# Optimization experiments

Measured on AMD Instinct MI355X. Metric: run time of the kernel, lower is better.

Reference implementation:

```python
import jax, jax.numpy as jnp
import numpy as np
import math

B, F, T = 32, 512, 4000
H, DK, DV = 8, 64, 64

def setup_inputs() -> dict:
    key = jax.random.key(0)
    ks = jax.random.split(key, 8)
    x = jax.random.normal(ks[0], (B, F, T), dtype=jnp.float32)
    weights = jax.random.randint(ks[1], (B, T), 0, 2, dtype=jnp.int32)
    # learned params
    q = jax.random.normal(ks[2], (H, DK), dtype=jnp.float32) / math.sqrt(DK)  # (1,H,1,dk) squeezed
    lim_k = 1.0 / math.sqrt(F)
    Wk = jax.random.uniform(ks[3], (H * DK, F), minval=-lim_k, maxval=lim_k, dtype=jnp.float32)
    bk = jax.random.uniform(ks[4], (H * DK,), minval=-lim_k, maxval=lim_k, dtype=jnp.float32)
    Wv = jax.random.uniform(ks[5], (H * DV, F), minval=-lim_k, maxval=lim_k, dtype=jnp.float32)
    bv = jax.random.uniform(ks[6], (H * DV,), minval=-lim_k, maxval=lim_k, dtype=jnp.float32)
    return {"x": x, "weights": weights, "q": q, "Wk": Wk, "bk": bk, "Wv": Wv, "bv": bv}

def reference(x, weights, q, Wk, bk, Wv, bv):
    # x: (B, F, T) -> transpose to (B, T, F) since dim=-1
    xt = jnp.swapaxes(x, 1, 2)                                  # (B,T,F)
    k = (xt @ Wk.T + bk).reshape(B, T, H, DK)                   # (B,T,H,dk)
    v = (xt @ Wv.T + bv).reshape(B, T, H, DV)                   # (B,T,H,dv)
    # scores: q (H,dk) dot k -> (B,H,T), scaled
    scores = jnp.einsum('hd,bthd->bht', q, k) / math.sqrt(DK)
    mask = (weights == 0)[:, None, :]                           # (B,1,T)
    scores = jnp.where(mask, jnp.float32(-1e30), scores)
    attn = jax.nn.softmax(scores, axis=-1)
    attn = jnp.where(mask, 0.0, attn)                           # (B,H,T)
    out = jnp.einsum('bht,bthv->bhv', attn, v)                  # (B,H,dv)
    return out.reshape(B, H * DV)                               # keepdim=False
```

## Files before the change

### kernel.cpp

```cpp
#include <hip/hip_runtime.h>
#include <math.h>

#define BB 32
#define FF 512
#define TT 4000
#define HH 8
#define DKK 64
#define DVV 64
#define NT4 1000

__global__ __launch_bounds__(256) void prep_qk(const float* __restrict__ q,
                                               const float* __restrict__ Wk,
                                               const float* __restrict__ bk,
                                               float* __restrict__ qk,
                                               float* __restrict__ qb) {
    int gid = blockIdx.x * 256 + threadIdx.x;
    int h = gid >> 9, f = gid & 511;
    float s = 0.f;
#pragma unroll 8
    for (int d = 0; d < DKK; ++d)
        s += q[h * DKK + d] * Wk[(size_t)(h * DKK + d) * FF + f];
    qk[gid] = s * 0.125f;
    if (gid < HH) {
        float sb = 0.f;
        for (int d = 0; d < DKK; ++d) sb += q[gid * DKK + d] * bk[gid * DKK + d];
        qb[gid] = sb * 0.125f;
    }
}

__global__ __launch_bounds__(256) void prep_wvt(const float* __restrict__ Wv,
                                                float* __restrict__ WvT) {
    int gid = blockIdx.x * 256 + threadIdx.x;
    int hv = gid >> 9, f = gid & 511;
    WvT[f * 512 + hv] = Wv[gid];
}

__global__ __launch_bounds__(256) void k_scores(const float* __restrict__ x,
                                                const float* __restrict__ qk,
                                                const float* __restrict__ qb,
                                                float* __restrict__ sc) {
    __shared__ float4 part[HH * 4 * 64];
    int b = blockIdx.y, tt = blockIdx.x;
    int tid = threadIdx.x, w = tid >> 6, l = tid & 63;
    int t0 = tt << 8;
    int t = t0 + (l << 2);
    float4 acc[HH];
#pragma unroll
    for (int h = 0; h < HH; ++h) acc[h] = make_float4(0.f, 0.f, 0.f, 0.f);
    if (t < TT) {
        const float* xp = x + (size_t)b * FF * TT + t;
        int f40 = w * 32;
        for (int f4 = f40; f4 < f40 + 32; ++f4) {
            int f = f4 << 2;
            float4 xv0 = *(const float4*)(xp + (size_t)(f + 0) * TT);
            float4 xv1 = *(const float4*)(xp + (size_t)(f + 1) * TT);
            float4 xv2 = *(const float4*)(xp + (size_t)(f + 2) * TT);
            float4 xv3 = *(const float4*)(xp + (size_t)(f + 3) * TT);
#pragma unroll
            for (int h = 0; h < HH; ++h) {
                float4 qv = *(const float4*)(qk + h * FF + f);
                acc[h].x += qv.x * xv0.x + qv.y * xv1.x + qv.z * xv2.x + qv.w * xv3.x;
                acc[h].y += qv.x * xv0.y + qv.y * xv1.y + qv.z * xv2.y + qv.w * xv3.y;
                acc[h].z += qv.x * xv0.z + qv.y * xv1.z + qv.z * xv2.z + qv.w * xv3.z;
                acc[h].w += qv.x * xv0.w + qv.y * xv1.w + qv.z * xv2.w + qv.w * xv3.w;
            }
        }
    }
#pragma unroll
    for (int h = 0; h < HH; ++h) part[(h * 4 + w) * 64 + l] = acc[h];
    __syncthreads();
    for (int p = tid; p < 512; p += 256) {
        int h = p >> 6, ll = p & 63;
        int t2 = t0 + (ll << 2);
        if (t2 >= TT) continue;
        float4 a0 = part[(h * 4 + 0) * 64 + ll];
        float4 a1 = part[(h * 4 + 1) * 64 + ll];
        float4 a2 = part[(h * 4 + 2) * 64 + ll];
        float4 a3 = part[(h * 4 + 3) * 64 + ll];
        float qbh = qb[h];
        float4 o;
        o.x = a0.x + a1.x + a2.x + a3.x + qbh;
        o.y = a0.y + a1.y + a2.y + a3.y + qbh;
        o.z = a0.z + a1.z + a2.z + a3.z + qbh;
        o.w = a0.w + a1.w + a2.w + a3.w + qbh;
        *(float4*)(sc + ((size_t)(b * HH + h)) * TT + t2) = o;
    }
}

__global__ __launch_bounds__(256) void k_softmax(float* __restrict__ sc,
                                                 const int* __restrict__ wts) {
    __shared__ float s4[4];
    int bh = blockIdx.x, b = bh >> 3;
    int tid = threadIdx.x, w = tid >> 6, l = tid & 63;
    float* row = sc + (size_t)bh * TT;
    const int* wr = wts + (size_t)b * TT;
    float4 v[4];
    float m = -3.0e38f;
#pragma unroll
    for (int k = 0; k < 4; ++k) {
        int i = tid + k * 256;
        if (i < NT4) {
            float4 s = *(const float4*)(row + (i << 2));
            int4 wv = *(const int4*)(wr + (i << 2));
            if (wv.x == 0) s.x = -1e30f;
            if (wv.y == 0) s.y = -1e30f;
            if (wv.z == 0) s.z = -1e30f;
            if (wv.w == 0) s.w = -1e30f;
            v[k] = s;
            m = fmaxf(m, fmaxf(fmaxf(s.x, s.y), fmaxf(s.z, s.w)));
        }
    }
#pragma unroll
    for (int d = 1; d < 64; d <<= 1) m = fmaxf(m, __shfl_xor(m, d));
    if (l == 0) s4[w] = m;
    __syncthreads();
    m = fmaxf(fmaxf(s4[0], s4[1]), fmaxf(s4[2], s4[3]));
    __syncthreads();
    float lsum = 0.f;
#pragma unroll
    for (int k = 0; k < 4; ++k) {
        int i = tid + k * 256;
        if (i < NT4) {
            float4 s = v[k];
            s.x = __expf(s.x - m);
            s.y = __expf(s.y - m);
            s.z = __expf(s.z - m);
            s.w = __expf(s.w - m);
            v[k] = s;
            lsum += s.x + s.y + s.z + s.w;
        }
    }
#pragma unroll
    for (int d = 1; d < 64; d <<= 1) lsum += __shfl_xor(lsum, d);
    if (l == 0) s4[w] = lsum;
    __syncthreads();
    lsum = s4[0] + s4[1] + s4[2] + s4[3];
    float inv = (m <= -1e29f) ? 0.f : (1.f / lsum);
#pragma unroll
    for (int k = 0; k < 4; ++k) {
        int i = tid + k * 256;
        if (i < NT4) {
            float4 s = v[k];
            s.x *= inv; s.y *= inv; s.z *= inv; s.w *= inv;
            *(float4*)(row + (i << 2)) = s;
        }
    }
}

__global__ __launch_bounds__(256) void k_y(const float* __restrict__ x,
                                           const float* __restrict__ attn,
                                           float* __restrict__ y) {
    __shared__ float red[32 * 257];
    int b = blockIdx.y, ft = blockIdx.x;
    int tid = threadIdx.x;
    int f0 = ft << 2;
    float acc[8][4];
#pragma unroll
    for (int h = 0; h < 8; ++h)
#pragma unroll
        for (int f = 0; f < 4; ++f) acc[h][f] = 0.f;
    const float* ab = attn + (size_t)b * HH * TT;
    const float* xb = x + ((size_t)b * FF + f0) * TT;
    for (int i = tid; i < NT4; i += 256) {
        int t = i << 2;
        float4 a[8];
#pragma unroll
        for (int h = 0; h < 8; ++h) a[h] = *(const float4*)(ab + (size_t)h * TT + t);
        float4 xv[4];
#pragma unroll
        for (int f = 0; f < 4; ++f) xv[f] = *(const float4*)(xb + (size_t)f * TT + t);
#pragma unroll
        for (int h = 0; h < 8; ++h)
#pragma unroll
            for (int f = 0; f < 4; ++f)
                acc[h][f] += a[h].x * xv[f].x + a[h].y * xv[f].y +
                             a[h].z * xv[f].z + a[h].w * xv[f].w;
    }
#pragma unroll
    for (int o = 0; o < 32; ++o) red[o * 257 + tid] = acc[o >> 2][o & 3];
    __syncthreads();
    if (tid < 32) {
        float vsum = 0.f;
        for (int j = 0; j < 256; ++j) vsum += red[tid * 257 + j];
        int h = tid >> 2, fo = tid & 3;
        y[((size_t)b * HH + h) * FF + f0 + fo] = vsum;
    }
}

__global__ __launch_bounds__(64) void k_out(const float* __restrict__ y,
                                            const float* __restrict__ WvT,
                                            const float* __restrict__ bv,
                                            float* __restrict__ out) {
    __shared__ float ys[FF];
    int h = blockIdx.x, b = blockIdx.y, tid = threadIdx.x;
    const float* yr = y + ((size_t)b * HH + h) * FF;
    for (int i = tid; i < FF; i += 64) ys[i] = yr[i];
    __syncthreads();
    float acc = 0.f;
    int hv = (h << 6) + tid;
    for (int f = 0; f < FF; ++f)
        acc += ys[f] * WvT[f * 512 + hv];
    out[b * 512 + hv] = acc + bv[hv];
}

extern "C" void kernel_launch(void* const* d_in, const int* in_sizes, int n_in,
                              void* d_out, int out_size, void* d_ws, size_t ws_size,
                              hipStream_t stream) {
    const float* x  = (const float*)d_in[0];
    const int*   wts = (const int*)d_in[1];
    const float* q  = (const float*)d_in[2];
    const float* Wk = (const float*)d_in[3];
    const float* bk = (const float*)d_in[4];
    const float* Wv = (const float*)d_in[5];
    const float* bv = (const float*)d_in[6];
    float* out = (float*)d_out;
    float* ws = (float*)d_ws;

    float* qk  = ws;
    float* qb  = ws + 4096;
    float* WvT = ws + 8192;
    float* sc  = ws + 270336;
    float* y   = ws + 1294336;

    prep_qk<<<16, 256, 0, stream>>>(q, Wk, bk, qk, qb);
    prep_wvt<<<1024, 256, 0, stream>>>(Wv, WvT);
    k_scores<<<dim3(16, 32), 256, 0, stream>>>(x, qk, qb, sc);
    k_softmax<<<256, 256, 0, stream>>>(sc, wts);
    k_y<<<dim3(128, 32), 256, 0, stream>>>(x, sc, y);
    k_out<<<dim3(8, 32), 64, 0, stream>>>(y, WvT, bv, out);
}
```

Baseline: 462.9 us.

## Process batches in groups so x stays cache-resident between scores and y passes

The score, softmax and weighted-sum kernels now run in two batch groups of 16 instead of over all 32 batches at once. The intent is that the x slice read by k_scores is still in the large last-level cache when k_y reads it again. The diff also tiles the Wv transpose through shared memory, replaces k_y's serial 256-element final reduction with a two-stage parallel one, and widens k_out to 256 threads per block. The cost is more kernel launches and smaller grids per launch (16x16 blocks for scores), which may underfill the GPU.

```diff
diff --git a/kernel.cpp b/kernel.cpp
--- a/kernel.cpp
+++ b/kernel.cpp
@@ -8,6 +8,7 @@
 #define DKK 64
 #define DVV 64
 #define NT4 1000
+#define GRP 16
 
 __global__ __launch_bounds__(256) void prep_qk(const float* __restrict__ q,
                                                const float* __restrict__ Wk,
@@ -30,17 +31,29 @@
 
 __global__ __launch_bounds__(256) void prep_wvt(const float* __restrict__ Wv,
                                                 float* __restrict__ WvT) {
-    int gid = blockIdx.x * 256 + threadIdx.x;
-    int hv = gid >> 9, f = gid & 511;
-    WvT[f * 512 + hv] = Wv[gid];
+    __shared__ float tile[64][65];
+    int hv0 = blockIdx.x * 64, f0 = blockIdx.y * 64;
+    int tj = threadIdx.x & 63, ti = threadIdx.x >> 6;
+#pragma unroll
+    for (int r = 0; r < 16; ++r) {
+        int i = ti * 16 + r;
+        tile[i][tj] = Wv[(size_t)(hv0 + i) * FF + f0 + tj];
+    }
+    __syncthreads();
+#pragma unroll
+    for (int r = 0; r < 16; ++r) {
+        int i = ti * 16 + r;
+        WvT[(size_t)(f0 + i) * FF + hv0 + tj] = tile[tj][i];
+    }
 }
 
 __global__ __launch_bounds__(256) void k_scores(const float* __restrict__ x,
                                                 const float* __restrict__ qk,
                                                 const float* __restrict__ qb,
-                                                float* __restrict__ sc) {
+                                                float* __restrict__ sc,
+                                                int b0) {
     __shared__ float4 part[HH * 4 * 64];
-    int b = blockIdx.y, tt = blockIdx.x;
+    int b = b0 + blockIdx.y, tt = blockIdx.x;
     int tid = threadIdx.x, w = tid >> 6, l = tid & 63;
     int t0 = tt << 8;
     int t = t0 + (l << 2);
@@ -88,9 +101,10 @@
 }
 
 __global__ __launch_bounds__(256) void k_softmax(float* __restrict__ sc,
-                                                 const int* __restrict__ wts) {
+                                                 const int* __restrict__ wts,
+                                                 int b0) {
     __shared__ float s4[4];
-    int bh = blockIdx.x, b = bh >> 3;
+    int bh = b0 * HH + blockIdx.x, b = bh >> 3;
     int tid = threadIdx.x, w = tid >> 6, l = tid & 63;
     float* row = sc + (size_t)bh * TT;
     const int* wr = wts + (size_t)b * TT;
@@ -149,9 +163,11 @@
 
 __global__ __launch_bounds__(256) void k_y(const float* __restrict__ x,
                                            const float* __restrict__ attn,
-                                           float* __restrict__ y) {
+                                           float* __restrict__ y,
+                                           int b0) {
     __shared__ float red[32 * 257];
-    int b = blockIdx.y, ft = blockIdx.x;
+    __shared__ float red2[32 * 8];
+    int b = b0 + blockIdx.y, ft = blockIdx.x;
     int tid = threadIdx.x;
     int f0 = ft << 2;
     float acc[8][4];
@@ -179,42 +195,55 @@
 #pragma unroll
     for (int o = 0; o < 32; ++o) red[o * 257 + tid] = acc[o >> 2][o & 3];
     __syncthreads();
+    {
+        int o = tid >> 3, seg = tid & 7;
+        float s = 0.f;
+#pragma unroll
+        for (int j = 0; j < 32; ++j) s += red[o * 257 + seg * 32 + j];
+        red2[o * 8 + seg] = s;
+    }
+    __syncthreads();
     if (tid < 32) {
         float vsum = 0.f;
-        for (int j = 0; j < 256; ++j) vsum += red[tid * 257 + j];
+#pragma unroll
+        for (int j = 0; j < 8; ++j) vsum += red2[tid * 8 + j];
         int h = tid >> 2, fo = tid & 3;
         y[((size_t)b * HH + h) * FF + f0 + fo] = vsum;
     }
 }
 
-__global__ __launch_bounds__(64) void k_out(const float* __restrict__ y,
-                                            const float* __restrict__ WvT,
-                                            const float* __restrict__ bv,
-                                            float* __restrict__ out) {
-    __shared__ float ys[FF];
-    int h = blockIdx.x, b = blockIdx.y, tid = threadIdx.x;
-    const float* yr = y + ((size_t)b * HH + h) * FF;
-    for (int i = tid; i < FF; i += 64) ys[i] = yr[i];
-    __syncthreads();
+__global__ __launch_bounds__(256) void k_out(const float* __restrict__ y,
+                                             const float* __restrict__ WvT,
+                                             const float* __restrict__ bv,
+                                             float* __restrict__ out) {
+    __shared__ float ys[4 * FF];
+    int half = blockIdx.x, b = blockIdx.y, tid = threadIdx.x;
+    int h0 = half * 4;
+    const float* yr = y + ((size_t)b * HH + h0) * FF;
+    for (int i = tid; i < 4 * FF; i += 256) ys[i] = yr[i];
+    __syncthreads();
+    int hv = half * 256 + tid;
+    int hloc = tid >> 6;
+    const float* ysr = ys + hloc * FF;
     float acc = 0.f;
-    int hv = (h << 6) + tid;
+#pragma unroll 8
     for (int f = 0; f < FF; ++f)
-        acc += ys[f] * WvT[f * 512 + hv];
+        acc += ysr[f] * WvT[(size_t)f * FF + hv];
     out[b * 512 + hv] = acc + bv[hv];
 }
 
 extern "C" void kernel_launch(void* const* d_in, const int* in_sizes, int n_in,
                               void* d_out, int out_size, void* d_ws, size_t ws_size,
                               hipStream_t stream) {
-    const float* x  = (const float*)d_in[0];
+    const float* x   = (const float*)d_in[0];
     const int*   wts = (const int*)d_in[1];
-    const float* q  = (const float*)d_in[2];
-    const float* Wk = (const float*)d_in[3];
-    const float* bk = (const float*)d_in[4];
-    const float* Wv = (const float*)d_in[5];
-    const float* bv = (const float*)d_in[6];
+    const float* q   = (const float*)d_in[2];
+    const float* Wk  = (const float*)d_in[3];
+    const float* bk  = (const float*)d_in[4];
+    const float* Wv  = (const float*)d_in[5];
+    const float* bv  = (const float*)d_in[6];
     float* out = (float*)d_out;
-    float* ws = (float*)d_ws;
+    float* ws  = (float*)d_ws;
 
     float* qk  = ws;
     float* qb  = ws + 4096;
@@ -223,9 +252,11 @@
     float* y   = ws + 1294336;
 
     prep_qk<<<16, 256, 0, stream>>>(q, Wk, bk, qk, qb);
-    prep_wvt<<<1024, 256, 0, stream>>>(Wv, WvT);
-    k_scores<<<dim3(16, 32), 256, 0, stream>>>(x, qk, qb, sc);
-    k_softmax<<<256, 256, 0, stream>>>(sc, wts);
-    k_y<<<dim3(128, 32), 256, 0, stream>>>(x, sc, y);
-    k_out<<<dim3(8, 32), 64, 0, stream>>>(y, WvT, bv, out);
-}
+    prep_wvt<<<dim3(8, 8), 256, 0, stream>>>(Wv, WvT);
+    for (int b0 = 0; b0 < BB; b0 += GRP) {
+        k_scores<<<dim3(16, GRP), 256, 0, stream>>>(x, qk, qb, sc, b0);
+        k_softmax<<<GRP * HH, 256, 0, stream>>>(sc, wts, b0);
+        k_y<<<dim3(128, GRP), 256, 0, stream>>>(x, sc, y, b0);
+    }
+    k_out<<<dim3(2, 32), 256, 0, stream>>>(y, WvT, bv, out);
+}
```

After: 466.7 us. No clear change (+0.8%).
